# Kernel optimization log

Measured on AMD Instinct MI355X. Metric: run time of the kernel, lower is better.

## Reference

```python
import jax, jax.numpy as jnp
import numpy as np

B, S, D = 4, 4096, 1024

def setup_inputs() -> dict:
    key = jax.random.key(0)
    k0, k1, k2, k3 = jax.random.split(key, 4)
    x = jax.random.normal(k0, (B, S, D), dtype=jnp.float32)
    # nn.Linear weights, applied as x @ W.T; init scaled ~1/sqrt(D)
    Wq = jax.random.normal(k1, (D, D), dtype=jnp.float32) / np.sqrt(D)
    Wk = jax.random.normal(k2, (D, D), dtype=jnp.float32) / np.sqrt(D)
    Wv = jax.random.normal(k3, (D, D), dtype=jnp.float32) / np.sqrt(D)
    return {"x": x, "Wq": Wq, "Wk": Wk, "Wv": Wv}

def reference(x, Wq, Wk, Wv):
    scale = x.shape[-1] ** (-0.5)
    Q = jnp.einsum('bsd,ed->bse', x, Wq)  # nn.Linear: x @ W.T
    K = jnp.einsum('bsd,ed->bse', x, Wk)
    V = jnp.einsum('bsd,ed->bse', x, Wv)
    scores = jax.nn.softmax(jnp.einsum('bqd,bkd->bqk', Q, K) * scale, axis=-1)
    return jnp.einsum('bqk,bkd->bqd', scores, V)
```

## Files before the change

kernel.cpp:

```cpp
#include <hip/hip_runtime.h>

typedef __bf16 bf16_t;
typedef bf16_t bf16x8 __attribute__((ext_vector_type(8)));
typedef float floatx4 __attribute__((ext_vector_type(4)));

#define BM 128
#define BN 128
#define BK 32

__device__ __forceinline__ void async_load16(const bf16_t* g, bf16_t* l) {
  __builtin_amdgcn_global_load_lds(
      (const __attribute__((address_space(1))) unsigned int*)g,
      (__attribute__((address_space(3))) unsigned int*)l, 16, 0, 0);
}

__device__ __forceinline__ int xcd_swizzle(int p, int total) {
  return (total % 8 == 0) ? (p & 7) * (total >> 3) + (p >> 3) : p;
}

__device__ __forceinline__ void gemm_acc(
    const bf16_t* __restrict__ A, const bf16_t* __restrict__ B,
    int K, int lda, int ldb, int bm, int bn, floatx4 (&acc)[4][4])
{
  __shared__ bf16_t lA[2][BM * BK];
  __shared__ bf16_t lB[2][BN * BK];
  const int t = threadIdx.x;
  const int lane = t & 63;
  const int wm = ((t >> 6) & 1) * 64;
  const int wn = (t >> 7) * 64;
  const int fr = lane & 15;
  const int fk = (((lane >> 4) ^ ((fr >> 1) & 3)) * 8);

  const int r0 = t >> 2;
  const int k0 = (((t & 3) ^ ((t >> 3) & 3)) * 8);
  const long aBase = (long)(bm + r0) * lda + k0;
  const long bBase = (long)(bn + r0) * ldb + k0;

  async_load16(A + aBase,                  &lA[0][t * 8]);
  async_load16(A + aBase + (long)64 * lda, &lA[0][2048 + t * 8]);
  async_load16(B + bBase,                  &lB[0][t * 8]);
  async_load16(B + bBase + (long)64 * ldb, &lB[0][2048 + t * 8]);

  int buf = 0;
  for (int kt = 0; kt < K; kt += BK) {
    __syncthreads();
    if (kt + BK < K) {
      const int nb = buf ^ 1;
      async_load16(A + aBase + kt + BK,                  &lA[nb][t * 8]);
      async_load16(A + aBase + (long)64 * lda + kt + BK, &lA[nb][2048 + t * 8]);
      async_load16(B + bBase + kt + BK,                  &lB[nb][t * 8]);
      async_load16(B + bBase + (long)64 * ldb + kt + BK, &lB[nb][2048 + t * 8]);
    }
    bf16x8 afr[4], bfr[4];
    #pragma unroll
    for (int i = 0; i < 4; ++i)
      afr[i] = *(const bf16x8*)&lA[buf][(wm + i * 16 + fr) * BK + fk];
    #pragma unroll
    for (int j = 0; j < 4; ++j)
      bfr[j] = *(const bf16x8*)&lB[buf][(wn + j * 16 + fr) * BK + fk];
    #pragma unroll
    for (int i = 0; i < 4; ++i)
      #pragma unroll
      for (int j = 0; j < 4; ++j)
        acc[i][j] = __builtin_amdgcn_mfma_f32_16x16x32_bf16(
            afr[i], bfr[j], acc[i][j], 0, 0, 0);
    buf ^= 1;
  }
}

template <typename OutT>
__device__ __forceinline__ void store_tile(
    OutT* __restrict__ C, int ldc, int bm, int bn,
    floatx4 (&acc)[4][4], float scale)
{
  const int t = threadIdx.x;
  const int lane = t & 63;
  const int wm = ((t >> 6) & 1) * 64;
  const int wn = (t >> 7) * 64;
  const int rq = (lane >> 4) * 4;
  const int c15 = lane & 15;
  #pragma unroll
  for (int i = 0; i < 4; ++i) {
    const int row0 = bm + wm + i * 16 + rq;
    #pragma unroll
    for (int j = 0; j < 4; ++j) {
      const int col = bn + wn + j * 16 + c15;
      #pragma unroll
      for (int r = 0; r < 4; ++r)
        C[(long)(row0 + r) * ldc + col] = (OutT)(acc[i][j][r] * scale);
    }
  }
}

__device__ __forceinline__ void decode_grid(int& z, int& by, int& bx) {
  const int gx = gridDim.x, gy = gridDim.y;
  const int total = gx * gy * gridDim.z;
  int P = ((int)blockIdx.z * gy + (int)blockIdx.y) * gx + (int)blockIdx.x;
  int L = xcd_swizzle(P, total);
  z = L / (gx * gy);
  const int rem = L - z * gx * gy;
  by = rem / gx;
  bx = rem - by * gx;
}

__global__ __launch_bounds__(256, 2) void gemm_qkv(
    const bf16_t* __restrict__ xb, const bf16_t* __restrict__ Wqb,
    const bf16_t* __restrict__ Wkb, const bf16_t* __restrict__ Wvb,
    bf16_t* __restrict__ Q, bf16_t* __restrict__ Kp, bf16_t* __restrict__ Vt)
{
  const int L = xcd_swizzle((int)blockIdx.x, 3072);
  const int z = L >> 10;
  const int r = L & 1023;
  const bf16_t *A, *B; bf16_t* C;
  int bm, bn, ldc;
  if (z == 0)      { A = xb;  B = Wqb; C = Q;  bm = (r >> 3) * BM; bn = (r & 7) * BN; ldc = 1024; }
  else if (z == 1) { A = xb;  B = Wkb; C = Kp; bm = (r >> 3) * BM; bn = (r & 7) * BN; ldc = 1024; }
  else             { A = Wvb; B = xb;  C = Vt; bm = (r & 7) * BM; bn = (r >> 3) * BN; ldc = 16384; }
  floatx4 acc[4][4] = {};
  gemm_acc(A, B, 1024, 1024, 1024, bm, bn, acc);
  store_tile<bf16_t>(C, ldc, bm, bn, acc, 1.0f);
}

__global__ __launch_bounds__(256, 2) void gemm_qk_exp(
    const bf16_t* __restrict__ A, const bf16_t* __restrict__ B,
    bf16_t* __restrict__ C, float* __restrict__ rowsum,
    int K, int lda, int ldb, int ldc,
    long sA, long sB, long sC, long sR, float scale)
{
  int z, by, bx;
  decode_grid(z, by, bx);
  A += (long)z * sA; B += (long)z * sB; C += (long)z * sC;
  rowsum += (long)z * sR;
  const int bm = by * BM, bn = bx * BN;
  floatx4 acc[4][4] = {};
  gemm_acc(A, B, K, lda, ldb, bm, bn, acc);

  const int t = threadIdx.x;
  const int lane = t & 63;
  const int wm = ((t >> 6) & 1) * 64;
  const int wn = (t >> 7) * 64;
  const int rq = (lane >> 4) * 4;
  const int c15 = lane & 15;
  #pragma unroll
  for (int i = 0; i < 4; ++i) {
    #pragma unroll
    for (int r = 0; r < 4; ++r) {
      const int row = bm + wm + i * 16 + rq + r;
      float psum = 0.f;
      #pragma unroll
      for (int j = 0; j < 4; ++j) {
        const float e = __expf(acc[i][j][r] * scale);
        const bf16_t h = (bf16_t)e;
        C[(long)row * ldc + bn + wn + j * 16 + c15] = h;
        psum += (float)h;
      }
      #pragma unroll
      for (int off = 8; off >= 1; off >>= 1)
        psum += __shfl_xor(psum, off, 16);
      if (c15 == 0) atomicAdd(&rowsum[row], psum);
    }
  }
}

__global__ __launch_bounds__(256, 2) void gemm_pv(
    const bf16_t* __restrict__ A, const bf16_t* __restrict__ B,
    float* __restrict__ C, const float* __restrict__ rowsum,
    int K, int lda, int ldb, int ldc,
    long sA, long sB, long sC, long sR)
{
  int z, by, bx;
  decode_grid(z, by, bx);
  A += (long)z * sA; B += (long)z * sB; C += (long)z * sC;
  rowsum += (long)z * sR;
  const int bm = by * BM, bn = bx * BN;
  floatx4 acc[4][4] = {};
  gemm_acc(A, B, K, lda, ldb, bm, bn, acc);

  const int t = threadIdx.x;
  const int lane = t & 63;
  const int wm = ((t >> 6) & 1) * 64;
  const int wn = (t >> 7) * 64;
  const int rq = (lane >> 4) * 4;
  const int c15 = lane & 15;
  #pragma unroll
  for (int i = 0; i < 4; ++i) {
    #pragma unroll
    for (int r = 0; r < 4; ++r) {
      const int row = bm + wm + i * 16 + rq + r;
      const float inv = 1.0f / rowsum[row];
      #pragma unroll
      for (int j = 0; j < 4; ++j)
        C[(long)row * ldc + bn + wn + j * 16 + c15] = acc[i][j][r] * inv;
    }
  }
}

__global__ __launch_bounds__(256) void cvt_f32_bf16(
    const float* __restrict__ in, bf16_t* __restrict__ out, long n,
    float* __restrict__ rowsum, int nrs)
{
  const int bid = blockIdx.x;
  if (rowsum && bid < 64) {
    const int k = bid * 256 + threadIdx.x;
    if (k < nrs) rowsum[k] = 0.f;
  }
  long i = ((long)bid * 256 + threadIdx.x) * 4;
  if (i + 3 < n) {
    float4 f = *(const float4*)&in[i];
    bf16_t o[4] = {(bf16_t)f.x, (bf16_t)f.y, (bf16_t)f.z, (bf16_t)f.w};
    *(ulong1*)&out[i] = *(ulong1*)o;
  }
}

__global__ __launch_bounds__(256) void cvt3_f32_bf16(
    const float* __restrict__ w0, const float* __restrict__ w1,
    const float* __restrict__ w2, bf16_t* __restrict__ o0,
    bf16_t* __restrict__ o1, bf16_t* __restrict__ o2)
{
  const float* in = (blockIdx.z == 0) ? w0 : (blockIdx.z == 1) ? w1 : w2;
  bf16_t* out = (blockIdx.z == 0) ? o0 : (blockIdx.z == 1) ? o1 : o2;
  long i = ((long)blockIdx.x * 256 + threadIdx.x) * 4;
  float4 f = *(const float4*)&in[i];
  bf16_t o[4] = {(bf16_t)f.x, (bf16_t)f.y, (bf16_t)f.z, (bf16_t)f.w};
  *(ulong1*)&out[i] = *(ulong1*)o;
}

extern "C" void kernel_launch(void* const* d_in, const int* in_sizes, int n_in,
                              void* d_out, int out_size, void* d_ws, size_t ws_size,
                              hipStream_t stream) {
  (void)in_sizes; (void)n_in; (void)out_size;
  const float* x  = (const float*)d_in[0];
  const float* Wq = (const float*)d_in[1];
  const float* Wk = (const float*)d_in[2];
  const float* Wv = (const float*)d_in[3];
  float* out = (float*)d_out;

  const long BS = 16384, D = 1024, S = 4096;
  const long SD = S * D;
  const long SS = S * S;

  bf16_t* base = (bf16_t*)d_ws;
  bf16_t* Sc  = base;
  bf16_t* xb  = base;
  bf16_t* Wqb = base + SS;
  bf16_t* Wkb = Wqb + D * D;
  bf16_t* Wvb = Wkb + D * D;

  auto need = [&](long scElems) {
    return (size_t)(scElems + 3 * SS) * 2 + (size_t)BS * 4;
  };
  int nsc; long scE;
  if      (ws_size >= need(4 * SS)) { nsc = 4; scE = 4 * SS; }
  else if (ws_size >= need(2 * SS)) { nsc = 2; scE = 2 * SS; }
  else                              { nsc = 1; scE = SS + 3 * D * D; }

  bf16_t* Q  = base + scE;
  bf16_t* Kp = Q + SS;
  bf16_t* Vt = Kp + SS;
  float* rowsum = (float*)(Vt + SS);

  dim3 blk(256);
  cvt_f32_bf16<<<dim3((BS * D) / 1024), blk, 0, stream>>>(
      x, xb, BS * D, rowsum, (int)BS);
  cvt3_f32_bf16<<<dim3((D * D) / 1024, 1, 3), blk, 0, stream>>>(
      Wq, Wk, Wv, Wqb, Wkb, Wvb);

  gemm_qkv<<<dim3(3072), blk, 0, stream>>>(xb, Wqb, Wkb, Wvb, Q, Kp, Vt);

  const float scale = 0.03125f;
  if (nsc == 4) {
    gemm_qk_exp<<<dim3(S / BN, S / BM, 4), blk, 0, stream>>>(
        Q, Kp, Sc, rowsum, (int)D, (int)D, (int)D, (int)S,
        SD, SD, SS, S, scale);
    gemm_pv<<<dim3(D / BN, S / BM, 4), blk, 0, stream>>>(
        Sc, Vt, out, rowsum, (int)S, (int)S, (int)BS, (int)D,
        SS, S, SD, S);
  } else if (nsc == 2) {
    for (int p = 0; p < 2; ++p) {
      const long b0 = 2 * p;
      gemm_qk_exp<<<dim3(S / BN, S / BM, 2), blk, 0, stream>>>(
          Q + b0 * SD, Kp + b0 * SD, Sc, rowsum + b0 * S,
          (int)D, (int)D, (int)D, (int)S, SD, SD, SS, S, scale);
      gemm_pv<<<dim3(D / BN, S / BM, 2), blk, 0, stream>>>(
          Sc, Vt + b0 * S, out + b0 * SD, rowsum + b0 * S,
          (int)S, (int)S, (int)BS, (int)D, SS, S, SD, S);
    }
  } else {
    for (int b = 0; b < 4; ++b) {
      gemm_qk_exp<<<dim3(S / BN, S / BM, 1), blk, 0, stream>>>(
          Q + (long)b * SD, Kp + (long)b * SD, Sc, rowsum + (long)b * S,
          (int)D, (int)D, (int)D, (int)S, 0, 0, 0, 0, scale);
      gemm_pv<<<dim3(D / BN, S / BM, 1), blk, 0, stream>>>(
          Sc, Vt + (long)b * S, out + (long)b * SD, rowsum + (long)b * S,
          (int)S, (int)S, (int)BS, (int)D, 0, 0, 0, 0);
    }
  }
}
```

Before: 582.1 us.

## Switch GEMMs to 256x256 tiles with 8 waves and quadrant-interleaved prefetch

Replaces the 128x128x32 tile GEMM core with a 256x256x64 tile run by 512 threads. Each wave computes four 64x32 sub-quadrants, and global-to-LDS async loads for the next stages are spread across the quadrant steps. Explicit vmcnt waits, raw s_barrier calls and s_setprio around the MFMA bursts keep loads and matrix math overlapped. The aim is more operand reuse per LDS byte and fewer global loads. In exchange it uses 128KB of LDS per block, which limits occupancy, and the grid has fewer blocks, which can hurt wave-quantisation balance for the smaller GEMMs.

```diff
diff --git a/kernel.cpp b/kernel.cpp
--- a/kernel.cpp
+++ b/kernel.cpp
@@ -4,9 +4,13 @@
 typedef bf16_t bf16x8 __attribute__((ext_vector_type(8)));
 typedef float floatx4 __attribute__((ext_vector_type(4)));
 
-#define BM 128
-#define BN 128
-#define BK 32
+#define VMCNT(n) asm volatile("s_waitcnt vmcnt(" #n ")" ::: "memory")
+
+__device__ __forceinline__ void wg_barrier() {
+  asm volatile("" ::: "memory");
+  __builtin_amdgcn_s_barrier();
+  asm volatile("" ::: "memory");
+}
 
 __device__ __forceinline__ void async_load16(const bf16_t* g, bf16_t* l) {
   __builtin_amdgcn_global_load_lds(
@@ -18,76 +22,86 @@
   return (total % 8 == 0) ? (p & 7) * (total >> 3) + (p >> 3) : p;
 }
 
-__device__ __forceinline__ void gemm_acc(
+__device__ __forceinline__ void gemm_acc256(
     const bf16_t* __restrict__ A, const bf16_t* __restrict__ B,
-    int K, int lda, int ldb, int bm, int bn, floatx4 (&acc)[4][4])
-{
-  __shared__ bf16_t lA[2][BM * BK];
-  __shared__ bf16_t lB[2][BN * BK];
+    int K, int lda, int ldb, int bm, int bn, floatx4 (&acc)[4][4][2])
+{
+  __shared__ bf16_t lA[2][16384];
+  __shared__ bf16_t lB[2][16384];
   const int t = threadIdx.x;
   const int lane = t & 63;
-  const int wm = ((t >> 6) & 1) * 64;
-  const int wn = (t >> 7) * 64;
+  const int w = t >> 6;
+  const int wm64 = (w & 1) * 64;
+  const int wn32 = (w >> 1) * 32;
   const int fr = lane & 15;
-  const int fk = (((lane >> 4) ^ ((fr >> 1) & 3)) * 8);
+  const int fk = ((lane >> 4) ^ ((fr >> 1) & 3)) * 8;
 
   const int r0 = t >> 2;
-  const int k0 = (((t & 3) ^ ((t >> 3) & 3)) * 8);
-  const long aBase = (long)(bm + r0) * lda + k0;
-  const long bBase = (long)(bn + r0) * ldb + k0;
-
-  async_load16(A + aBase,                  &lA[0][t * 8]);
-  async_load16(A + aBase + (long)64 * lda, &lA[0][2048 + t * 8]);
-  async_load16(B + bBase,                  &lB[0][t * 8]);
-  async_load16(B + bBase + (long)64 * ldb, &lB[0][2048 + t * 8]);
-
-  int buf = 0;
-  for (int kt = 0; kt < K; kt += BK) {
-    __syncthreads();
-    if (kt + BK < K) {
-      const int nb = buf ^ 1;
-      async_load16(A + aBase + kt + BK,                  &lA[nb][t * 8]);
-      async_load16(A + aBase + (long)64 * lda + kt + BK, &lA[nb][2048 + t * 8]);
-      async_load16(B + bBase + kt + BK,                  &lB[nb][t * 8]);
-      async_load16(B + bBase + (long)64 * ldb + kt + BK, &lB[nb][2048 + t * 8]);
-    }
-    bf16x8 afr[4], bfr[4];
+  const int ksw = ((t & 3) ^ ((r0 >> 1) & 3)) * 8;
+  const long aRow = (long)(bm + r0) * lda + ksw;
+  const long bRow = (long)(bn + r0) * ldb + ksw;
+  const int NT = K >> 6;
+
+  auto stageA = [&](int buf, int h, int u) {
+    const bf16_t* s = A + aRow + (long)h * 128 * lda + u * 64;
+    bf16_t* d = &lA[buf][h * 4096 + t * 8];
+    async_load16(s, d);
+    async_load16(s + 32, d + 8192);
+  };
+  auto stageB = [&](int buf, int h, int u) {
+    const bf16_t* s = B + bRow + (long)h * 128 * ldb + u * 64;
+    bf16_t* d = &lB[buf][h * 4096 + t * 8];
+    async_load16(s, d);
+    async_load16(s + 32, d + 8192);
+  };
+
+  stageA(0, 0, 0);
+  stageB(0, 0, 0);
+  stageB(0, 1, 0);
+  stageA(0, 1, 0);
+  stageA(1, 0, 1);
+  stageB(1, 0, 1);
+  VMCNT(4);
+  wg_barrier();
+
+  for (int u = 0; u < NT; ++u) {
+    const int b = u & 1;
     #pragma unroll
-    for (int i = 0; i < 4; ++i)
-      afr[i] = *(const bf16x8*)&lA[buf][(wm + i * 16 + fr) * BK + fk];
-    #pragma unroll
-    for (int j = 0; j < 4; ++j)
-      bfr[j] = *(const bf16x8*)&lB[buf][(wn + j * 16 + fr) * BK + fk];
-    #pragma unroll
-    for (int i = 0; i < 4; ++i)
-      #pragma unroll
-      for (int j = 0; j < 4; ++j)
-        acc[i][j] = __builtin_amdgcn_mfma_f32_16x16x32_bf16(
-            afr[i], bfr[j], acc[i][j], 0, 0, 0);
-    buf ^= 1;
-  }
-}
-
-template <typename OutT>
-__device__ __forceinline__ void store_tile(
-    OutT* __restrict__ C, int ldc, int bm, int bn,
-    floatx4 (&acc)[4][4], float scale)
-{
-  const int t = threadIdx.x;
-  const int lane = t & 63;
-  const int wm = ((t >> 6) & 1) * 64;
-  const int wn = (t >> 7) * 64;
-  const int rq = (lane >> 4) * 4;
-  const int c15 = lane & 15;
-  #pragma unroll
-  for (int i = 0; i < 4; ++i) {
-    const int row0 = bm + wm + i * 16 + rq;
-    #pragma unroll
-    for (int j = 0; j < 4; ++j) {
-      const int col = bn + wn + j * 16 + c15;
-      #pragma unroll
-      for (int r = 0; r < 4; ++r)
-        C[(long)(row0 + r) * ldc + col] = (OutT)(acc[i][j][r] * scale);
+    for (int q = 0; q < 4; ++q) {
+      const int mh = q >> 1, nh = q & 1;
+      bf16x8 af[2][4], bf[2][2];
+      #pragma unroll
+      for (int kk = 0; kk < 2; ++kk) {
+        #pragma unroll
+        for (int i = 0; i < 4; ++i)
+          af[kk][i] = *(const bf16x8*)
+              &lA[b][kk * 8192 + (mh * 128 + wm64 + i * 16 + fr) * 32 + fk];
+        #pragma unroll
+        for (int j = 0; j < 2; ++j)
+          bf[kk][j] = *(const bf16x8*)
+              &lB[b][kk * 8192 + (nh * 128 + wn32 + j * 16 + fr) * 32 + fk];
+      }
+      if (q == 0)      { if (u + 1 < NT) stageB(b ^ 1, 1, u + 1); }
+      else if (q == 1) { if (u + 1 < NT) stageA(b ^ 1, 1, u + 1); }
+      else if (q == 2) { if (u + 2 < NT) stageA(b, 0, u + 2); }
+      else             { if (u + 2 < NT) stageB(b, 0, u + 2); }
+      wg_barrier();
+      __builtin_amdgcn_s_setprio(1);
+      #pragma unroll
+      for (int i = 0; i < 4; ++i)
+        #pragma unroll
+        for (int j = 0; j < 2; ++j) {
+          acc[q][i][j] = __builtin_amdgcn_mfma_f32_16x16x32_bf16(
+              af[0][i], bf[0][j], acc[q][i][j], 0, 0, 0);
+          acc[q][i][j] = __builtin_amdgcn_mfma_f32_16x16x32_bf16(
+              af[1][i], bf[1][j], acc[q][i][j], 0, 0, 0);
+        }
+      __builtin_amdgcn_s_setprio(0);
+      if (q == 3) {
+        if (u < NT - 2)       { VMCNT(4); }
+        else if (u == NT - 2) { VMCNT(0); }
+      }
+      wg_barrier();
     }
   }
 }
@@ -103,25 +117,45 @@
   bx = rem - by * gx;
 }
 
-__global__ __launch_bounds__(256, 2) void gemm_qkv(
+__global__ __launch_bounds__(512, 2) void gemm_qkv(
     const bf16_t* __restrict__ xb, const bf16_t* __restrict__ Wqb,
     const bf16_t* __restrict__ Wkb, const bf16_t* __restrict__ Wvb,
     bf16_t* __restrict__ Q, bf16_t* __restrict__ Kp, bf16_t* __restrict__ Vt)
 {
-  const int L = xcd_swizzle((int)blockIdx.x, 3072);
-  const int z = L >> 10;
-  const int r = L & 1023;
+  const int L = xcd_swizzle((int)blockIdx.x, 768);
+  const int z = L >> 8;
+  const int r = L & 255;
   const bf16_t *A, *B; bf16_t* C;
   int bm, bn, ldc;
-  if (z == 0)      { A = xb;  B = Wqb; C = Q;  bm = (r >> 3) * BM; bn = (r & 7) * BN; ldc = 1024; }
-  else if (z == 1) { A = xb;  B = Wkb; C = Kp; bm = (r >> 3) * BM; bn = (r & 7) * BN; ldc = 1024; }
-  else             { A = Wvb; B = xb;  C = Vt; bm = (r & 7) * BM; bn = (r >> 3) * BN; ldc = 16384; }
-  floatx4 acc[4][4] = {};
-  gemm_acc(A, B, 1024, 1024, 1024, bm, bn, acc);
-  store_tile<bf16_t>(C, ldc, bm, bn, acc, 1.0f);
-}
-
-__global__ __launch_bounds__(256, 2) void gemm_qk_exp(
+  if (z == 0)      { A = xb;  B = Wqb; C = Q;  bm = (r >> 2) * 256; bn = (r & 3) * 256; ldc = 1024; }
+  else if (z == 1) { A = xb;  B = Wkb; C = Kp; bm = (r >> 2) * 256; bn = (r & 3) * 256; ldc = 1024; }
+  else             { A = Wvb; B = xb;  C = Vt; bm = (r & 3) * 256; bn = (r >> 2) * 256; ldc = 16384; }
+  floatx4 acc[4][4][2] = {};
+  gemm_acc256(A, B, 1024, 1024, 1024, bm, bn, acc);
+
+  const int t = threadIdx.x;
+  const int lane = t & 63;
+  const int w = t >> 6;
+  const int wm64 = (w & 1) * 64;
+  const int wn32 = (w >> 1) * 32;
+  const int rq = (lane >> 4) * 4;
+  const int c15 = lane & 15;
+  #pragma unroll
+  for (int q = 0; q < 4; ++q) {
+    const int rB = bm + (q >> 1) * 128 + wm64;
+    const int cB = bn + (q & 1) * 128 + wn32;
+    #pragma unroll
+    for (int i = 0; i < 4; ++i)
+      #pragma unroll
+      for (int j = 0; j < 2; ++j)
+        #pragma unroll
+        for (int r = 0; r < 4; ++r)
+          C[(long)(rB + i * 16 + rq + r) * ldc + cB + j * 16 + c15] =
+              (bf16_t)acc[q][i][j][r];
+  }
+}
+
+__global__ __launch_bounds__(512, 2) void gemm_qk_exp(
     const bf16_t* __restrict__ A, const bf16_t* __restrict__ B,
     bf16_t* __restrict__ C, float* __restrict__ rowsum,
     int K, int lda, int ldb, int ldc,
@@ -131,38 +165,44 @@
   decode_grid(z, by, bx);
   A += (long)z * sA; B += (long)z * sB; C += (long)z * sC;
   rowsum += (long)z * sR;
-  const int bm = by * BM, bn = bx * BN;
-  floatx4 acc[4][4] = {};
-  gemm_acc(A, B, K, lda, ldb, bm, bn, acc);
+  const int bm = by * 256, bn = bx * 256;
+  floatx4 acc[4][4][2] = {};
+  gemm_acc256(A, B, K, lda, ldb, bm, bn, acc);
 
   const int t = threadIdx.x;
   const int lane = t & 63;
-  const int wm = ((t >> 6) & 1) * 64;
-  const int wn = (t >> 7) * 64;
+  const int w = t >> 6;
+  const int wm64 = (w & 1) * 64;
+  const int wn32 = (w >> 1) * 32;
   const int rq = (lane >> 4) * 4;
   const int c15 = lane & 15;
   #pragma unroll
-  for (int i = 0; i < 4; ++i) {
+  for (int q = 0; q < 4; ++q) {
+    const int rB = bm + (q >> 1) * 128 + wm64;
+    const int cB = bn + (q & 1) * 128 + wn32;
     #pragma unroll
-    for (int r = 0; r < 4; ++r) {
-      const int row = bm + wm + i * 16 + rq + r;
-      float psum = 0.f;
-      #pragma unroll
-      for (int j = 0; j < 4; ++j) {
-        const float e = __expf(acc[i][j][r] * scale);
-        const bf16_t h = (bf16_t)e;
-        C[(long)row * ldc + bn + wn + j * 16 + c15] = h;
-        psum += (float)h;
+    for (int i = 0; i < 4; ++i) {
+      #pragma unroll
+      for (int r = 0; r < 4; ++r) {
+        const int row = rB + i * 16 + rq + r;
+        float psum = 0.f;
+        #pragma unroll
+        for (int j = 0; j < 2; ++j) {
+          const float e = __expf(acc[q][i][j][r] * scale);
+          const bf16_t h = (bf16_t)e;
+          C[(long)row * ldc + cB + j * 16 + c15] = h;
+          psum += (float)h;
+        }
+        #pragma unroll
+        for (int off = 8; off >= 1; off >>= 1)
+          psum += __shfl_xor(psum, off, 16);
+        if (c15 == 0) atomicAdd(&rowsum[row], psum);
       }
-      #pragma unroll
-      for (int off = 8; off >= 1; off >>= 1)
-        psum += __shfl_xor(psum, off, 16);
-      if (c15 == 0) atomicAdd(&rowsum[row], psum);
-    }
-  }
-}
-
-__global__ __launch_bounds__(256, 2) void gemm_pv(
+    }
+  }
+}
+
+__global__ __launch_bounds__(512, 2) void gemm_pv(
     const bf16_t* __restrict__ A, const bf16_t* __restrict__ B,
     float* __restrict__ C, const float* __restrict__ rowsum,
     int K, int lda, int ldb, int ldc,
@@ -172,25 +212,31 @@
   decode_grid(z, by, bx);
   A += (long)z * sA; B += (long)z * sB; C += (long)z * sC;
   rowsum += (long)z * sR;
-  const int bm = by * BM, bn = bx * BN;
-  floatx4 acc[4][4] = {};
-  gemm_acc(A, B, K, lda, ldb, bm, bn, acc);
+  const int bm = by * 256, bn = bx * 256;
+  floatx4 acc[4][4][2] = {};
+  gemm_acc256(A, B, K, lda, ldb, bm, bn, acc);
 
   const int t = threadIdx.x;
   const int lane = t & 63;
-  const int wm = ((t >> 6) & 1) * 64;
-  const int wn = (t >> 7) * 64;
+  const int w = t >> 6;
+  const int wm64 = (w & 1) * 64;
+  const int wn32 = (w >> 1) * 32;
   const int rq = (lane >> 4) * 4;
   const int c15 = lane & 15;
   #pragma unroll
-  for (int i = 0; i < 4; ++i) {
+  for (int q = 0; q < 4; ++q) {
+    const int rB = bm + (q >> 1) * 128 + wm64;
+    const int cB = bn + (q & 1) * 128 + wn32;
     #pragma unroll
-    for (int r = 0; r < 4; ++r) {
-      const int row = bm + wm + i * 16 + rq + r;
-      const float inv = 1.0f / rowsum[row];
-      #pragma unroll
-      for (int j = 0; j < 4; ++j)
-        C[(long)row * ldc + bn + wn + j * 16 + c15] = acc[i][j][r] * inv;
+    for (int i = 0; i < 4; ++i) {
+      #pragma unroll
+      for (int r = 0; r < 4; ++r) {
+        const int row = rB + i * 16 + rq + r;
+        const float inv = 1.0f / rowsum[row];
+        #pragma unroll
+        for (int j = 0; j < 2; ++j)
+          C[(long)row * ldc + cB + j * 16 + c15] = acc[q][i][j][r] * inv;
+      }
     }
   }
 }
@@ -259,38 +305,38 @@
   bf16_t* Vt = Kp + SS;
   float* rowsum = (float*)(Vt + SS);
 
-  dim3 blk(256);
+  dim3 blk(256), blk512(512);
   cvt_f32_bf16<<<dim3((BS * D) / 1024), blk, 0, stream>>>(
       x, xb, BS * D, rowsum, (int)BS);
   cvt3_f32_bf16<<<dim3((D * D) / 1024, 1, 3), blk, 0, stream>>>(
       Wq, Wk, Wv, Wqb, Wkb, Wvb);
 
-  gemm_qkv<<<dim3(3072), blk, 0, stream>>>(xb, Wqb, Wkb, Wvb, Q, Kp, Vt);
+  gemm_qkv<<<dim3(768), blk512, 0, stream>>>(xb, Wqb, Wkb, Wvb, Q, Kp, Vt);
 
   const float scale = 0.03125f;
   if (nsc == 4) {
-    gemm_qk_exp<<<dim3(S / BN, S / BM, 4), blk, 0, stream>>>(
+    gemm_qk_exp<<<dim3(16, 16, 4), blk512, 0, stream>>>(
         Q, Kp, Sc, rowsum, (int)D, (int)D, (int)D, (int)S,
         SD, SD, SS, S, scale);
-    gemm_pv<<<dim3(D / BN, S / BM, 4), blk, 0, stream>>>(
+    gemm_pv<<<dim3(4, 16, 4), blk512, 0, stream>>>(
         Sc, Vt, out, rowsum, (int)S, (int)S, (int)BS, (int)D,
         SS, S, SD, S);
   } else if (nsc == 2) {
     for (int p = 0; p < 2; ++p) {
       const long b0 = 2 * p;
-      gemm_qk_exp<<<dim3(S / BN, S / BM, 2), blk, 0, stream>>>(
+      gemm_qk_exp<<<dim3(16, 16, 2), blk512, 0, stream>>>(
           Q + b0 * SD, Kp + b0 * SD, Sc, rowsum + b0 * S,
           (int)D, (int)D, (int)D, (int)S, SD, SD, SS, S, scale);
-      gemm_pv<<<dim3(D / BN, S / BM, 2), blk, 0, stream>>>(
+      gemm_pv<<<dim3(4, 16, 2), blk512, 0, stream>>>(
           Sc, Vt + b0 * S, out + b0 * SD, rowsum + b0 * S,
           (int)S, (int)S, (int)BS, (int)D, SS, S, SD, S);
     }
   } else {
     for (int b = 0; b < 4; ++b) {
-      gemm_qk_exp<<<dim3(S / BN, S / BM, 1), blk, 0, stream>>>(
+      gemm_qk_exp<<<dim3(16, 16, 1), blk512, 0, stream>>>(
           Q + (long)b * SD, Kp + (long)b * SD, Sc, rowsum + (long)b * S,
           (int)D, (int)D, (int)D, (int)S, 0, 0, 0, 0, scale);
-      gemm_pv<<<dim3(D / BN, S / BM, 1), blk, 0, stream>>>(
+      gemm_pv<<<dim3(4, 16, 1), blk512, 0, stream>>>(
           Sc, Vt + (long)b * S, out + (long)b * SD, rowsum + (long)b * S,
           (int)S, (int)S, (int)BS, (int)D, 0, 0, 0, 0);
     }
```

Result: slower. 691.0 us (+18.7%).
